# Performance work log

Hardware: AMD Instinct MI355X
Metric: run time of the kernel (lower is better)

The kernel has to match this reference:

```python
import jax, jax.numpy as jnp
import numpy as np

H = 16  # n_head

def _rotate_half(x):
    d = x.shape[-1] // 2
    return jnp.concatenate([-x[..., d:], x[..., :d]], axis=-1)

def setup_inputs() -> dict:
    key = jax.random.key(0)
    ks = jax.random.split(key, 12)
    b, t, f, h = 8, 1024, 1024, H
    d = f // h
    inp = {
        "query": jax.random.normal(ks[0], (b, t, f), jnp.float32),
        "key": jax.random.normal(ks[1], (b, t, f), jnp.float32),
        "value": jax.random.normal(ks[2], (b, t, f), jnp.float32),
    }
    # realistic rotary cos/sin, shape (t,1,1,d_k)
    inv_freq = 1.0 / (10000.0 ** (np.arange(0, d, 2, dtype=np.float32) / d))
    pos = np.arange(t, dtype=np.float32)[:, None] * inv_freq[None, :]  # (t, d/2)
    emb = np.concatenate([pos, pos], axis=-1)  # (t, d)
    inp["cos"] = jnp.asarray(np.cos(emb)).reshape(t, 1, 1, d)
    inp["sin"] = jnp.asarray(np.sin(emb)).reshape(t, 1, 1, d)
    inp["mask"] = jax.random.randint(ks[3], (b, t, t), 0, 2) > 0
    s = 1.0 / np.sqrt(f)
    inp["Wq"] = jax.random.normal(ks[4], (f, f), jnp.float32) * s
    inp["bq"] = jax.random.normal(ks[5], (f,), jnp.float32) * 0.02
    inp["Wk"] = jax.random.normal(ks[6], (f, f), jnp.float32) * s
    inp["bk"] = jax.random.normal(ks[7], (f,), jnp.float32) * 0.02
    inp["Wv"] = jax.random.normal(ks[8], (f, f), jnp.float32) * s
    inp["bv"] = jax.random.normal(ks[9], (f,), jnp.float32) * 0.02
    inp["Wo"] = jax.random.normal(ks[10], (f, f), jnp.float32) * s
    inp["bo"] = jax.random.normal(ks[11], (f,), jnp.float32) * 0.02
    return inp

def reference(query, key, value, cos, sin, mask, Wq, bq, Wk, bk, Wv, bv, Wo, bo):
    b, t, f = query.shape
    h = H
    d = f // h
    # RoPE applied pre-projection, per-head layout (b,t,h,d)
    c = cos.reshape(1, t, 1, d)  # broadcast over batch and heads
    s = sin.reshape(1, t, 1, d)
    qr = query.reshape(b, t, h, d)
    kr = key.reshape(b, t, h, d)
    qr = qr * c + _rotate_half(qr) * s
    kr = kr * c + _rotate_half(kr) * s
    q_in = qr.reshape(b, t, f)
    k_in = kr.reshape(b, t, f)
    # QKV projections (nn.Linear: x @ W.T + b), then split heads -> (b,h,t,d)
    q = (jnp.einsum('btf,gf->btg', q_in, Wq) + bq).reshape(b, t, h, d).transpose(0, 2, 1, 3)
    k = (jnp.einsum('btf,gf->btg', k_in, Wk) + bk).reshape(b, t, h, d).transpose(0, 2, 1, 3)
    v = (jnp.einsum('btf,gf->btg', value, Wv) + bv).reshape(b, t, h, d).transpose(0, 2, 1, 3)
    scores = jnp.einsum('bhqd,bhkd->bhqk', q, k) / jnp.sqrt(jnp.asarray(d, q.dtype))
    m = mask[:, None, :, :]  # (b,1,t,t)
    scores = jnp.where(m, jnp.asarray(-10000.0, scores.dtype), scores)
    attn = jax.nn.softmax(scores, axis=-1)
    attn = jnp.where(m, jnp.asarray(0.0, attn.dtype), attn)
    out = jnp.einsum('bhqk,bhkd->bhqd', attn, v)  # (b,h,t,d)
    out = out.transpose(0, 2, 1, 3).reshape(b, t, f)
    return jnp.einsum('btf,gf->btg', out, Wo) + bo
```

## Files before the change

### kernel.cpp

```cpp
#include <hip/hip_runtime.h>
#include <stdint.h>

typedef short short8 __attribute__((ext_vector_type(8)));
typedef float f32x4 __attribute__((ext_vector_type(4)));
typedef unsigned short ushort4v __attribute__((ext_vector_type(4)));
typedef unsigned int uint4v __attribute__((ext_vector_type(4)));
typedef unsigned long long u64;

#if __has_builtin(__builtin_amdgcn_exp2f)
#define EXP2(x) __builtin_amdgcn_exp2f(x)
#else
#define EXP2(x) exp2f(x)
#endif

__device__ __forceinline__ unsigned short f2bf(float f) {
  union { float f; unsigned u; } v; v.f = f;
  unsigned r = v.u + 0x7fffu + ((v.u >> 16) & 1u);
  return (unsigned short)(r >> 16);
}

__device__ __forceinline__ unsigned cvt_pk_bf16(float lo, float hi) {
  unsigned r;
  asm("v_cvt_pk_bf16_f32 %0, %1, %2" : "=v"(r) : "v"(lo), "v"(hi));
  return r;
}

__device__ __forceinline__ void gld_lds16(const void* g, void* l) {
  __builtin_amdgcn_global_load_lds((const __attribute__((address_space(1))) void*)g,
                                   (__attribute__((address_space(3))) void*)l, 16, 0, 0);
}

__global__ void prep_kernel(const float* __restrict__ q, const float* __restrict__ k,
                            const float* __restrict__ v,
                            const float* __restrict__ cs, const float* __restrict__ sn,
                            unsigned short* __restrict__ qo, unsigned short* __restrict__ ko,
                            unsigned short* __restrict__ vo,
                            const int* __restrict__ mask, u64* __restrict__ bits,
                            const float* __restrict__ s0, const float* __restrict__ s1,
                            const float* __restrict__ s2, const float* __restrict__ s3,
                            unsigned short* __restrict__ d0, unsigned short* __restrict__ d1,
                            unsigned short* __restrict__ d2, unsigned short* __restrict__ d3) {
  const int bx = blockIdx.x;
  if (bx < 4096) {
    const int idx = bx * 256 + threadIdx.x;
    const int p   = idx & 7;
    const int bth = idx >> 3;
    const int t   = (bth >> 4) & 1023;
    const size_t base = (size_t)bth * 64;
    const int dd0 = p * 4;

    const float4 x0 = *(const float4*)(q + base + dd0);
    const float4 x1 = *(const float4*)(q + base + dd0 + 32);
    const float4 y0 = *(const float4*)(k + base + dd0);
    const float4 y1 = *(const float4*)(k + base + dd0 + 32);
    const float4 c0 = *(const float4*)(cs + t * 64 + dd0);
    const float4 c1 = *(const float4*)(cs + t * 64 + dd0 + 32);
    const float4 sl = *(const float4*)(sn + t * 64 + dd0);
    const float4 sh = *(const float4*)(sn + t * 64 + dd0 + 32);

    ushort4v qlo, qhi, klo, khi;
    qlo[0]=f2bf(x0.x*c0.x - x1.x*sl.x); qlo[1]=f2bf(x0.y*c0.y - x1.y*sl.y);
    qlo[2]=f2bf(x0.z*c0.z - x1.z*sl.z); qlo[3]=f2bf(x0.w*c0.w - x1.w*sl.w);
    qhi[0]=f2bf(x1.x*c1.x + x0.x*sh.x); qhi[1]=f2bf(x1.y*c1.y + x0.y*sh.y);
    qhi[2]=f2bf(x1.z*c1.z + x0.z*sh.z); qhi[3]=f2bf(x1.w*c1.w + x0.w*sh.w);
    klo[0]=f2bf(y0.x*c0.x - y1.x*sl.x); klo[1]=f2bf(y0.y*c0.y - y1.y*sl.y);
    klo[2]=f2bf(y0.z*c0.z - y1.z*sl.z); klo[3]=f2bf(y0.w*c0.w - y1.w*sl.w);
    khi[0]=f2bf(y1.x*c1.x + y0.x*sh.x); khi[1]=f2bf(y1.y*c1.y + y0.y*sh.y);
    khi[2]=f2bf(y1.z*c1.z + y0.z*sh.z); khi[3]=f2bf(y1.w*c1.w + y0.w*sh.w);

    *(ushort4v*)(qo + base + dd0)      = qlo;
    *(ushort4v*)(qo + base + dd0 + 32) = qhi;
    *(ushort4v*)(ko + base + dd0)      = klo;
    *(ushort4v*)(ko + base + dd0 + 32) = khi;

    const size_t vb = (size_t)idx * 8;
    const float4 va = *(const float4*)(v + vb);
    const float4 vbv = *(const float4*)(v + vb + 4);
    ushort4v oa, ob;
    oa[0]=f2bf(va.x); oa[1]=f2bf(va.y); oa[2]=f2bf(va.z); oa[3]=f2bf(va.w);
    ob[0]=f2bf(vbv.x); ob[1]=f2bf(vbv.y); ob[2]=f2bf(vbv.z); ob[3]=f2bf(vbv.w);
    *(ushort4v*)(vo + vb)     = oa;
    *(ushort4v*)(vo + vb + 4) = ob;
  } else if (bx < 36864) {
    const int tid = (bx - 4096) * 256 + threadIdx.x;
    const int w = tid >> 6, j = tid & 63;
    const int gh = w & 1, ktb = (w >> 1) & 7, bq = w >> 4;
    const int nt = (j >> 2) & 7, r = j & 3, g = gh * 2 + (j >> 5);
    const int kk = nt * 16 + g * 4 + r;
    const int mv = mask[(size_t)bq * 1024 + ktb * 128 + kk];
    const u64 b = __ballot(mv != 0);
    if (j == 0) bits[w] = b;
  } else {
    const int idx2 = bx - 36864;
    const int m = idx2 >> 10;
    const float* src = (m == 0) ? s0 : (m == 1) ? s1 : (m == 2) ? s2 : s3;
    unsigned short* dst = (m == 0) ? d0 : (m == 1) ? d1 : (m == 2) ? d2 : d3;
    const int i = (idx2 & 1023) * 256 + threadIdx.x;
    const float4 vv = *(const float4*)(src + (size_t)i * 4);
    ushort4v o;
    o[0]=f2bf(vv.x); o[1]=f2bf(vv.y); o[2]=f2bf(vv.z); o[3]=f2bf(vv.w);
    *(ushort4v*)(dst + (size_t)i * 4) = o;
  }
}

__global__ __launch_bounds__(256, 4) void gemm_qkv(
    const unsigned short* __restrict__ Aq, const unsigned short* __restrict__ Ak,
    const unsigned short* __restrict__ Av,
    const unsigned short* __restrict__ Bq, const unsigned short* __restrict__ Bk,
    const unsigned short* __restrict__ Bv,
    const float* __restrict__ bq, const float* __restrict__ bk, const float* __restrict__ bv,
    unsigned short* __restrict__ Cq, unsigned short* __restrict__ Ck,
    unsigned short* __restrict__ Cv) {
  constexpr int K = 1024;
  const int z = blockIdx.z;
  const unsigned short* A  = (z == 0) ? Aq : (z == 1) ? Ak : Av;
  const unsigned short* Bw = (z == 0) ? Bq : (z == 1) ? Bk : Bv;
  const float* bias        = (z == 0) ? bq : (z == 1) ? bk : bv;
  unsigned short* Co       = (z == 0) ? Cq : (z == 1) ? Ck : Cv;
  const float scale = (z == 0) ? 0.18033688f : 1.0f;

  const int tid = threadIdx.x;
  const int wave = tid >> 6, lane = tid & 63;
  const int m0 = blockIdx.x * 128, n0 = blockIdx.y * 128;
  __shared__ unsigned short Asm[128 * 64];
  __shared__ unsigned short Bsm[128 * 64];
  f32x4 acc[4][4] = {};
  const int wr = (wave >> 1) * 64, wc = (wave & 1) * 64;
  const int ld_row = lane >> 3;
  const int ld_col = ((lane & 7) ^ ld_row) * 8;
  const int fr = lane & 15, g = lane >> 4;
  const int fr7 = fr & 7;

  for (int k0 = 0; k0 < K; k0 += 64) {
#pragma unroll
    for (int j = 0; j < 4; ++j) {
      const int c = j * 4 + wave;
      gld_lds16(A  + (size_t)(m0 + 8 * c + ld_row) * K + k0 + ld_col, &Asm[c * 512]);
      gld_lds16(Bw + (size_t)(n0 + 8 * c + ld_row) * K + k0 + ld_col, &Bsm[c * 512]);
    }
    __syncthreads();
#pragma unroll
    for (int ks = 0; ks < 2; ++ks) {
      const int ch = ((ks * 4 + g) ^ fr7) * 8;
      short8 af[4], bf[4];
#pragma unroll
      for (int i = 0; i < 4; ++i)
        af[i] = *(const short8*)&Asm[(wr + i * 16 + fr) * 64 + ch];
#pragma unroll
      for (int i = 0; i < 4; ++i)
        bf[i] = *(const short8*)&Bsm[(wc + i * 16 + fr) * 64 + ch];
#pragma unroll
      for (int i = 0; i < 4; ++i)
#pragma unroll
        for (int j = 0; j < 4; ++j)
          acc[i][j] = __builtin_amdgcn_mfma_f32_16x16x32_bf16(af[i], bf[j], acc[i][j], 0, 0, 0);
    }
    __syncthreads();
  }

#pragma unroll
  for (int i = 0; i < 4; ++i) {
    const int row_base = m0 + wr + i * 16 + g * 4;
#pragma unroll
    for (int j = 0; j < 4; ++j) {
      const int col = n0 + wc + j * 16 + fr;
      const float bval = bias[col];
      const int h_i = col >> 6, dd = col & 63;
      if (z < 2) {
#pragma unroll
        for (int r = 0; r < 4; ++r) {
          const int row = row_base + r;
          const int b_i = row >> 10, t_i = row & 1023;
          Co[((size_t)(b_i * 16 + h_i) * 1024 + t_i) * 64 + dd] = f2bf((acc[i][j][r] + bval) * scale);
        }
      } else {
#pragma unroll
        for (int r = 0; r < 4; ++r) {
          const int row = row_base + r;
          const int b_i = row >> 10, t_i = row & 1023;
          const int kk = t_i & 127;
          const int kp = ((kk >> 4) & 3) * 32 + ((kk >> 2) & 3) * 8 + ((kk >> 6) & 1) * 4 + (kk & 3);
          Co[((size_t)(b_i * 16 + h_i) * 64 + dd) * 1024 + (t_i & ~127) + kp] =
              f2bf((acc[i][j][r] + bval));
        }
      }
    }
  }
}

__global__ __launch_bounds__(256, 4) void gemm_o(
    const unsigned short* __restrict__ A, const unsigned short* __restrict__ Bw,
    const float* __restrict__ bias, float* __restrict__ C) {
  constexpr int K = 1024, N = 1024;
  const int tid = threadIdx.x;
  const int wave = tid >> 6, lane = tid & 63;
  const int m0 = blockIdx.x * 128, n0 = blockIdx.y * 128;
  __shared__ unsigned short Asm[128 * 64];
  __shared__ unsigned short Bsm[128 * 64];
  f32x4 acc[4][4] = {};
  const int wr = (wave >> 1) * 64, wc = (wave & 1) * 64;
  const int ld_row = lane >> 3;
  const int ld_col = ((lane & 7) ^ ld_row) * 8;
  const int fr = lane & 15, g = lane >> 4;
  const int fr7 = fr & 7;

  for (int k0 = 0; k0 < K; k0 += 64) {
#pragma unroll
    for (int j = 0; j < 4; ++j) {
      const int c = j * 4 + wave;
      gld_lds16(A  + (size_t)(m0 + 8 * c + ld_row) * K + k0 + ld_col, &Asm[c * 512]);
      gld_lds16(Bw + (size_t)(n0 + 8 * c + ld_row) * K + k0 + ld_col, &Bsm[c * 512]);
    }
    __syncthreads();
#pragma unroll
    for (int ks = 0; ks < 2; ++ks) {
      const int ch = ((ks * 4 + g) ^ fr7) * 8;
      short8 af[4], bf[4];
#pragma unroll
      for (int i = 0; i < 4; ++i)
        af[i] = *(const short8*)&Asm[(wr + i * 16 + fr) * 64 + ch];
#pragma unroll
      for (int i = 0; i < 4; ++i)
        bf[i] = *(const short8*)&Bsm[(wc + i * 16 + fr) * 64 + ch];
#pragma unroll
      for (int i = 0; i < 4; ++i)
#pragma unroll
        for (int j = 0; j < 4; ++j)
          acc[i][j] = __builtin_amdgcn_mfma_f32_16x16x32_bf16(af[i], bf[j], acc[i][j], 0, 0, 0);
    }
    __syncthreads();
  }

#pragma unroll
  for (int i = 0; i < 4; ++i) {
    const int row_base = m0 + wr + i * 16 + g * 4;
#pragma unroll
    for (int j = 0; j < 4; ++j) {
      const int col = n0 + wc + j * 16 + fr;
      const float bval = bias[col];
#pragma unroll
      for (int r = 0; r < 4; ++r)
        C[(size_t)(row_base + r) * N + col] = acc[i][j][r] + bval;
    }
  }
}

__global__ __launch_bounds__(256, 2) void flash_attn(
    const unsigned short* __restrict__ Qp, const unsigned short* __restrict__ Kp,
    const unsigned short* __restrict__ Vp, const u64* __restrict__ mbits,
    unsigned short* __restrict__ O) {
  const int bh = blockIdx.x & 127, b_i = bh >> 4, h_i = bh & 15;
  const int q0 = (blockIdx.x >> 7) * 128;
  const int tid = threadIdx.x, wave = tid >> 6, lane = tid & 63;
  const unsigned short* Qb = Qp + (size_t)bh * 65536;
  const unsigned short* Kb = Kp + (size_t)bh * 65536;
  const unsigned short* Vb = Vp + (size_t)bh * 65536;
  const u64* mb = mbits + (size_t)b_i * 16384;

  __shared__ unsigned short smem[32768];

  const int fr = lane & 15, g = lane >> 4, fr7 = fr & 7;
  const int qw = q0 + wave * 32;

  short8 qf[2][2];
#pragma unroll
  for (int mt = 0; mt < 2; ++mt)
#pragma unroll
    for (int ks = 0; ks < 2; ++ks)
      qf[mt][ks] = *(const short8*)&Qb[(size_t)(qw + mt * 16 + fr) * 64 + ks * 32 + g * 8];

  f32x4 o_acc[2][4] = {};
  f32x4 o_l[2] = {};
  const short8 ones = {0x3F80, 0x3F80, 0x3F80, 0x3F80, 0x3F80, 0x3F80, 0x3F80, 0x3F80};

  const int kld_row = lane >> 3;
  const int kld_col = ((lane & 7) ^ kld_row) * 8;
  const int vld_row = lane >> 4;
  const int vld_r7w = 4 * (wave & 1) + vld_row;
  const int vld_col = ((lane & 15) ^ vld_r7w) * 8;

#define STAGE(P, KT)                                                                     \
  do {                                                                                   \
    _Pragma("unroll")                                                                    \
    for (int j = 0; j < 4; ++j) {                                                        \
      const int c = j * 4 + wave;                                                        \
      gld_lds16(Kb + (size_t)((KT) + 8 * c + kld_row) * 64 + kld_col,                    \
                &smem[(P) * 16384 + 8192 + c * 512]);                                    \
      gld_lds16(Vb + (size_t)(4 * c + vld_row) * 1024 + (KT) + vld_col,                  \
                &smem[(P) * 16384 + c * 512]);                                           \
    }                                                                                    \
  } while (0)

  STAGE(0, 0);
  int p = 0;
  for (int kt = 0; kt < 1024; kt += 128) {
    if (kt < 896) {
      STAGE(p ^ 1, kt + 128);
      asm volatile("s_waitcnt vmcnt(8)" ::: "memory");
    } else {
      asm volatile("s_waitcnt vmcnt(0)" ::: "memory");
    }
    __builtin_amdgcn_s_barrier();
    asm volatile("" ::: "memory");
    const unsigned short* Vsm = &smem[p * 16384];
    const unsigned short* Ksm = &smem[p * 16384 + 8192];

    const u64 w0 = mb[(size_t)(qw + fr) * 16 + (kt >> 7) * 2 + (g >> 1)];
    const u64 w1 = mb[(size_t)(qw + 16 + fr) * 16 + (kt >> 7) * 2 + (g >> 1)];

    f32x4 s_acc[2][8] = {};
#pragma unroll
    for (int ks = 0; ks < 2; ++ks) {
      const int ch = ((ks * 4 + g) ^ fr7) * 8;
      short8 kf[8];
#pragma unroll
      for (int nt = 0; nt < 8; ++nt)
        kf[nt] = *(const short8*)&Ksm[(nt * 16 + fr) * 64 + ch];
      __builtin_amdgcn_s_setprio(1);
#pragma unroll
      for (int mt = 0; mt < 2; ++mt)
#pragma unroll
        for (int nt = 0; nt < 8; ++nt)
          s_acc[mt][nt] = __builtin_amdgcn_mfma_f32_16x16x32_bf16(kf[nt], qf[mt][ks], s_acc[mt][nt], 0, 0, 0);
      __builtin_amdgcn_s_setprio(0);
    }

    short8 pf[2][4];
#pragma unroll
    for (int mt = 0; mt < 2; ++mt) {
      const u64 w = mt ? w1 : w0;
      const unsigned bits = (unsigned)(w >> ((g & 1) * 32));
#pragma unroll
      for (int ks2 = 0; ks2 < 4; ++ks2) {
        float e[8];
#pragma unroll
        for (int r = 0; r < 4; ++r) {
          float a = EXP2(s_acc[mt][ks2][r]);
          a = (bits & (1u << (ks2 * 4 + r))) ? 0.0f : a;
          float b2 = EXP2(s_acc[mt][ks2 + 4][r]);
          b2 = (bits & (1u << (16 + ks2 * 4 + r))) ? 0.0f : b2;
          e[r] = a; e[4 + r] = b2;
        }
        uint4v pk;
        pk[0] = cvt_pk_bf16(e[0], e[1]);
        pk[1] = cvt_pk_bf16(e[2], e[3]);
        pk[2] = cvt_pk_bf16(e[4], e[5]);
        pk[3] = cvt_pk_bf16(e[6], e[7]);
        union { uint4v u; short8 s; } cv; cv.u = pk;
        pf[mt][ks2] = cv.s;
      }
    }

#pragma unroll
    for (int ks2 = 0; ks2 < 4; ++ks2) {
      const int cc = (ks2 * 4 + g) ^ fr7;
      short8 vf[4];
#pragma unroll
      for (int dt = 0; dt < 4; ++dt)
        vf[dt] = *(const short8*)&Vsm[(dt * 16 + fr) * 128 + cc * 8];
      __builtin_amdgcn_s_setprio(1);
#pragma unroll
      for (int mt = 0; mt < 2; ++mt) {
#pragma unroll
        for (int dt = 0; dt < 4; ++dt)
          o_acc[mt][dt] = __builtin_amdgcn_mfma_f32_16x16x32_bf16(pf[mt][ks2], vf[dt], o_acc[mt][dt], 0, 0, 0);
        o_l[mt] = __builtin_amdgcn_mfma_f32_16x16x32_bf16(pf[mt][ks2], ones, o_l[mt], 0, 0, 0);
      }
      __builtin_amdgcn_s_setprio(0);
    }
    asm volatile("" ::: "memory");
    __builtin_amdgcn_s_barrier();
    p ^= 1;
  }
#undef STAGE

#pragma unroll
  for (int mt = 0; mt < 2; ++mt) {
#pragma unroll
    for (int r = 0; r < 4; ++r) {
      const float inv_l = 1.0f / o_l[mt][r];
      const int qrow = qw + mt * 16 + g * 4 + r;
#pragma unroll
      for (int dt = 0; dt < 4; ++dt) {
        const int dcol = dt * 16 + fr;
        O[((size_t)(b_i * 1024 + qrow)) * 1024 + h_i * 64 + dcol] = f2bf(o_acc[mt][dt][r] * inv_l);
      }
    }
  }
}

extern "C" void kernel_launch(void* const* d_in, const int* in_sizes, int n_in,
                              void* d_out, int out_size, void* d_ws, size_t ws_size,
                              hipStream_t stream) {
  const float* query = (const float*)d_in[0];
  const float* key   = (const float*)d_in[1];
  const float* value = (const float*)d_in[2];
  const float* cosb  = (const float*)d_in[3];
  const float* sinb  = (const float*)d_in[4];
  const int*   mask  = (const int*)d_in[5];
  const float* Wq = (const float*)d_in[6];
  const float* bq = (const float*)d_in[7];
  const float* Wk = (const float*)d_in[8];
  const float* bk = (const float*)d_in[9];
  const float* Wv = (const float*)d_in[10];
  const float* bv = (const float*)d_in[11];
  const float* Wo = (const float*)d_in[12];
  const float* bo = (const float*)d_in[13];
  (void)in_sizes; (void)n_in; (void)out_size; (void)ws_size;

  char* ws = (char*)d_ws;
  const size_t MB = 1024 * 1024;
  unsigned short* q_in = (unsigned short*)(ws);
  unsigned short* k_in = (unsigned short*)(ws + 16 * MB);
  unsigned short* v_bf = (unsigned short*)(ws + 32 * MB);
  unsigned short* Qp   = (unsigned short*)(ws + 48 * MB);
  unsigned short* Kp   = (unsigned short*)(ws + 64 * MB);
  unsigned short* Vp   = (unsigned short*)(ws + 80 * MB);
  unsigned short* Wqb  = (unsigned short*)(ws + 96 * MB);
  unsigned short* Wkb  = (unsigned short*)(ws + 98 * MB);
  unsigned short* Wvb  = (unsigned short*)(ws + 100 * MB);
  unsigned short* Wob  = (unsigned short*)(ws + 102 * MB);
  u64*            mbits= (u64*)(ws + 104 * MB);
  unsigned short* attn = q_in;

  prep_kernel<<<40960, 256, 0, stream>>>(query, key, value, cosb, sinb, q_in, k_in, v_bf,
                                         mask, mbits, Wq, Wk, Wv, Wo, Wqb, Wkb, Wvb, Wob);

  dim3 blk(256);
  gemm_qkv<<<dim3(64, 8, 3), blk, 0, stream>>>(q_in, k_in, v_bf, Wqb, Wkb, Wvb,
                                               bq, bk, bv, Qp, Kp, Vp);
  flash_attn<<<1024, blk, 0, stream>>>(Qp, Kp, Vp, mbits, attn);
  gemm_o<<<dim3(64, 8), blk, 0, stream>>>(attn, Wob, bo, (float*)d_out);
}
```

Before: 345.9 us.

## Pack mask bits with vectorized loads and prefetch mask words in attention

The mask-to-bitmask pass now has each wave read a full mask row with 16-byte int4 loads. It builds nibbles, combines them through LDS and compresses them into 64-bit words in natural column order. This replaces the per-element ballot layout and cuts the prep grid from 40960 to 10240 blocks. The attention kernel adapts its bit indexing to the new layout and prefetches the next tile's two mask words as a 128-bit load before the PV stage, hiding the latency of that load. The cost is more bit manipulation per element and a changed bit layout that the two kernels must keep consistent.

New measurement: 337.1 us. 2.6% less time.

```diff
diff --git a/kernel.cpp b/kernel.cpp
--- a/kernel.cpp
+++ b/kernel.cpp
@@ -6,6 +6,7 @@
 typedef unsigned short ushort4v __attribute__((ext_vector_type(4)));
 typedef unsigned int uint4v __attribute__((ext_vector_type(4)));
 typedef unsigned long long u64;
+typedef u64 u64x2 __attribute__((ext_vector_type(2)));
 
 #if __has_builtin(__builtin_amdgcn_exp2f)
 #define EXP2(x) __builtin_amdgcn_exp2f(x)
@@ -28,6 +29,13 @@
 __device__ __forceinline__ void gld_lds16(const void* g, void* l) {
   __builtin_amdgcn_global_load_lds((const __attribute__((address_space(1))) void*)g,
                                    (__attribute__((address_space(3))) void*)l, 16, 0, 0);
+}
+
+__device__ __forceinline__ unsigned nib_compress(u64 x) {
+  x = (x | (x >> 4))  & 0x00FF00FF00FF00FFull;
+  x = (x | (x >> 8))  & 0x0000FFFF0000FFFFull;
+  x = (x | (x >> 16));
+  return (unsigned)x;
 }
 
 __global__ void prep_kernel(const float* __restrict__ q, const float* __restrict__ k,
@@ -40,6 +48,7 @@
                             const float* __restrict__ s2, const float* __restrict__ s3,
                             unsigned short* __restrict__ d0, unsigned short* __restrict__ d1,
                             unsigned short* __restrict__ d2, unsigned short* __restrict__ d3) {
+  __shared__ unsigned mlds[256];
   const int bx = blockIdx.x;
   if (bx < 4096) {
     const int idx = bx * 256 + threadIdx.x;
@@ -81,17 +90,26 @@
     ob[0]=f2bf(vbv.x); ob[1]=f2bf(vbv.y); ob[2]=f2bf(vbv.z); ob[3]=f2bf(vbv.w);
     *(ushort4v*)(vo + vb)     = oa;
     *(ushort4v*)(vo + vb + 4) = ob;
-  } else if (bx < 36864) {
-    const int tid = (bx - 4096) * 256 + threadIdx.x;
-    const int w = tid >> 6, j = tid & 63;
-    const int gh = w & 1, ktb = (w >> 1) & 7, bq = w >> 4;
-    const int nt = (j >> 2) & 7, r = j & 3, g = gh * 2 + (j >> 5);
-    const int kk = nt * 16 + g * 4 + r;
-    const int mv = mask[(size_t)bq * 1024 + ktb * 128 + kk];
-    const u64 b = __ballot(mv != 0);
-    if (j == 0) bits[w] = b;
+  } else if (bx < 6144) {
+    const int wave = threadIdx.x >> 6, lane = threadIdx.x & 63;
+    const int mrow = (bx - 4096) * 4 + wave;
+    const int* mp = mask + (size_t)mrow * 1024 + lane * 16;
+    const int4 a0 = *(const int4*)(mp);
+    const int4 a1 = *(const int4*)(mp + 4);
+    const int4 a2 = *(const int4*)(mp + 8);
+    const int4 a3 = *(const int4*)(mp + 12);
+    const unsigned n0 = (a0.x!=0?1u:0u)|(a0.y!=0?2u:0u)|(a0.z!=0?4u:0u)|(a0.w!=0?8u:0u);
+    const unsigned n1 = (a1.x!=0?1u:0u)|(a1.y!=0?2u:0u)|(a1.z!=0?4u:0u)|(a1.w!=0?8u:0u);
+    const unsigned n2 = (a2.x!=0?1u:0u)|(a2.y!=0?2u:0u)|(a2.z!=0?4u:0u)|(a2.w!=0?8u:0u);
+    const unsigned n3 = (a3.x!=0?1u:0u)|(a3.y!=0?2u:0u)|(a3.z!=0?4u:0u)|(a3.w!=0?8u:0u);
+    mlds[wave * 64 + lane] = n0 | (n1 << 8) | (n2 << 16) | (n3 << 24);
+    if (lane < 16) {
+      const u64x2 x = ((const u64x2*)mlds)[wave * 16 + lane];
+      const u64 w = (u64)nib_compress(x[0]) | ((u64)nib_compress(x[1]) << 32);
+      bits[(size_t)mrow * 16 + lane] = w;
+    }
   } else {
-    const int idx2 = bx - 36864;
+    const int idx2 = bx - 6144;
     const int m = idx2 >> 10;
     const float* src = (m == 0) ? s0 : (m == 1) ? s1 : (m == 2) ? s2 : s3;
     unsigned short* dst = (m == 0) ? d0 : (m == 1) ? d1 : (m == 2) ? d2 : d3;
@@ -260,6 +278,7 @@
   __shared__ unsigned short smem[32768];
 
   const int fr = lane & 15, g = lane >> 4, fr7 = fr & 7;
+  const int shg = g * 4;
   const int qw = q0 + wave * 32;
 
   short8 qf[2][2];
@@ -291,6 +310,8 @@
     }                                                                                    \
   } while (0)
 
+  u64x2 wv0 = *(const u64x2*)&mb[(size_t)(qw + fr) * 16];
+  u64x2 wv1 = *(const u64x2*)&mb[(size_t)(qw + 16 + fr) * 16];
   STAGE(0, 0);
   int p = 0;
   for (int kt = 0; kt < 1024; kt += 128) {
@@ -305,9 +326,6 @@
     const unsigned short* Vsm = &smem[p * 16384];
     const unsigned short* Ksm = &smem[p * 16384 + 8192];
 
-    const u64 w0 = mb[(size_t)(qw + fr) * 16 + (kt >> 7) * 2 + (g >> 1)];
-    const u64 w1 = mb[(size_t)(qw + 16 + fr) * 16 + (kt >> 7) * 2 + (g >> 1)];
-
     f32x4 s_acc[2][8] = {};
 #pragma unroll
     for (int ks = 0; ks < 2; ++ks) {
@@ -328,17 +346,17 @@
     short8 pf[2][4];
 #pragma unroll
     for (int mt = 0; mt < 2; ++mt) {
-      const u64 w = mt ? w1 : w0;
-      const unsigned bits = (unsigned)(w >> ((g & 1) * 32));
+      const u64 sa = (mt ? wv1[0] : wv0[0]) >> shg;
+      const u64 sb = (mt ? wv1[1] : wv0[1]) >> shg;
 #pragma unroll
       for (int ks2 = 0; ks2 < 4; ++ks2) {
         float e[8];
 #pragma unroll
         for (int r = 0; r < 4; ++r) {
           float a = EXP2(s_acc[mt][ks2][r]);
-          a = (bits & (1u << (ks2 * 4 + r))) ? 0.0f : a;
+          a = ((unsigned)(sa >> (ks2 * 16 + r)) & 1u) ? 0.0f : a;
           float b2 = EXP2(s_acc[mt][ks2 + 4][r]);
-          b2 = (bits & (1u << (16 + ks2 * 4 + r))) ? 0.0f : b2;
+          b2 = ((unsigned)(sb >> (ks2 * 16 + r)) & 1u) ? 0.0f : b2;
           e[r] = a; e[4 + r] = b2;
         }
         uint4v pk;
@@ -349,6 +367,12 @@
         union { uint4v u; short8 s; } cv; cv.u = pk;
         pf[mt][ks2] = cv.s;
       }
+    }
+
+    {
+      const int ktn = (kt + 128) & 1023;
+      wv0 = *(const u64x2*)&mb[(size_t)(qw + fr) * 16 + (ktn >> 6)];
+      wv1 = *(const u64x2*)&mb[(size_t)(qw + 16 + fr) * 16 + (ktn >> 6)];
     }
 
 #pragma unroll
@@ -423,7 +447,7 @@
   u64*            mbits= (u64*)(ws + 104 * MB);
   unsigned short* attn = q_in;
 
-  prep_kernel<<<40960, 256, 0, stream>>>(query, key, value, cosb, sinb, q_in, k_in, v_bf,
+  prep_kernel<<<10240, 256, 0, stream>>>(query, key, value, cosb, sinb, q_in, k_in, v_bf,
                                          mask, mbits, Wq, Wk, Wv, Wo, Wqb, Wkb, Wvb, Wob);
 
   dim3 blk(256);
```
